# Performance work log

Hardware: AMD Instinct MI355X
Metric: run time of the kernel (lower is better)

Reference implementation:

```python
import jax, jax.numpy as jnp
import numpy as np

N_NODES = 50000
EPS = 1e-5


def sage_conv_max(x, src, dst, W_l, b_l, W_r):
    # PyG SAGEConv(aggr='max'): out = lin_l(max_j x_j) + lin_r(x_i)
    msg = x[src]                                   # [E, d] gather
    agg = jnp.full((x.shape[0], x.shape[1]), -jnp.inf, dtype=x.dtype)
    agg = agg.at[dst].max(msg)                     # scatter-max over edges
    agg = jnp.where(jnp.isneginf(agg), 0.0, agg)   # isolated nodes -> 0 (PyG convention)
    return agg @ W_l.T + b_l + x @ W_r.T


def batch_norm(x, gamma, beta):
    mean = jnp.mean(x, axis=0)
    var = jnp.var(x, axis=0)
    return (x - mean) * jax.lax.rsqrt(var + EPS) * gamma + beta


def setup_inputs() -> dict:
    key = jax.random.key(0)
    ks = jax.random.split(key, 10)
    d_in, d_h, d_out = 128, 128, 32
    s = lambda fan: 1.0 / np.sqrt(fan)
    return {
        "x": jax.random.normal(ks[0], (N_NODES, d_in), dtype=jnp.float32),
        "edge_index": jax.random.randint(ks[1], (2, 800000), 0, N_NODES, dtype=jnp.int32),
        "W_l1": jax.random.uniform(ks[2], (d_h, d_in), jnp.float32, -s(d_in), s(d_in)),
        "b_l1": jnp.zeros((d_h,), jnp.float32),
        "W_r1": jax.random.uniform(ks[3], (d_h, d_in), jnp.float32, -s(d_in), s(d_in)),
        "gamma1": jnp.ones((d_h,), jnp.float32),
        "beta1": jnp.zeros((d_h,), jnp.float32),
        "W_l2": jax.random.uniform(ks[4], (d_out, d_h), jnp.float32, -s(d_h), s(d_h)),
        "b_l2": jnp.zeros((d_out,), jnp.float32),
        "W_r2": jax.random.uniform(ks[5], (d_out, d_h), jnp.float32, -s(d_h), s(d_h)),
    }


def reference(x, edge_index, W_l1, b_l1, W_r1, gamma1, beta1, W_l2, b_l2, W_r2):
    src, dst = edge_index[0], edge_index[1]
    h = sage_conv_max(x, src, dst, W_l1, b_l1, W_r1)
    h = batch_norm(h, gamma1, beta1)
    h = jax.nn.relu(h)
    # dropout is identity at inference
    return sage_conv_max(h, src, dst, W_l2, b_l2, W_r2)
```

## Files before the change

kernel.cpp:

```cpp
#include <hip/hip_runtime.h>
#include <math.h>
#include <float.h>

#define N_NODES 50000
#define N_EDGES 800000
#define DH 128
#define NB 196
#define EB 4096
#define NBUCK 98
#define BSH 9
#define NTOT (NBUCK * NB)

typedef __attribute__((ext_vector_type(8))) short bf16x8;
typedef __attribute__((ext_vector_type(4))) float f32x4;

static __device__ __forceinline__ unsigned short f2bf(float f) {
  unsigned int u = __float_as_uint(f);
  u = (u + 0x7fff + ((u >> 16) & 1)) >> 16;
  return (unsigned short)u;
}

__global__ __launch_bounds__(256) void part_hist(const int* __restrict__ dst,
                                                 int* __restrict__ histT) {
  __shared__ int lh[NBUCK];
  const int tid = threadIdx.x, blk = blockIdx.x;
  if (tid < NBUCK) lh[tid] = 0;
  __syncthreads();
#pragma unroll
  for (int it = 0; it < EB / 256; ++it) {
    int e = blk * EB + it * 256 + tid;
    if (e < N_EDGES) atomicAdd(&lh[dst[e] >> BSH], 1);
  }
  __syncthreads();
  if (tid < NBUCK) histT[tid * NB + blk] = lh[tid];
}

__global__ __launch_bounds__(1024) void part_scan(int* __restrict__ histT) {
  const int PER = (NTOT + 1023) / 1024;
  int t = threadIdx.x;
  int v[(NTOT + 1023) / 1024];
  int base_i = t * PER;
  int mysum = 0;
#pragma unroll
  for (int i = 0; i < PER; ++i) {
    int idx = base_i + i;
    v[i] = (idx < NTOT) ? histT[idx] : 0;
    mysum += v[i];
  }
  __shared__ int s[1024];
  s[t] = mysum;
  __syncthreads();
  for (int off = 1; off < 1024; off <<= 1) {
    int x = (t >= off) ? s[t - off] : 0;
    __syncthreads();
    s[t] += x;
    __syncthreads();
  }
  int run = s[t] - mysum;
#pragma unroll
  for (int i = 0; i < PER; ++i) {
    int idx = base_i + i;
    if (idx < NTOT) histT[idx] = run;
    run += v[i];
  }
}

__global__ __launch_bounds__(256) void part_scatter(const int* __restrict__ src,
                                                    const int* __restrict__ dst,
                                                    const int* __restrict__ basesT,
                                                    unsigned int* __restrict__ pairs) {
  __shared__ int cur[NBUCK];
  const int tid = threadIdx.x, blk = blockIdx.x;
  if (tid < NBUCK) cur[tid] = basesT[tid * NB + blk];
  __syncthreads();
#pragma unroll
  for (int it = 0; it < EB / 256; ++it) {
    int e = blk * EB + it * 256 + tid;
    if (e < N_EDGES) {
      int d = dst[e];
      int p = atomicAdd(&cur[d >> BSH], 1);
      pairs[p] = (unsigned)src[e] | ((unsigned)(d & 511) << 16);
    }
  }
}

__global__ __launch_bounds__(1024) void bucket_sort(const unsigned int* __restrict__ pairs,
                                                    const int* __restrict__ basesT,
                                                    int* __restrict__ row_ptr,
                                                    int* __restrict__ elist) {
  __shared__ int hist[512], sc[512], cpos[512];
  const int b = blockIdx.x, tid = threadIdx.x;
  const int p0 = basesT[b * NB];
  const int p1 = (b < NBUCK - 1) ? basesT[(b + 1) * NB] : N_EDGES;
  if (tid < 512) hist[tid] = 0;
  __syncthreads();
  for (int p = p0 + tid; p < p1; p += 1024)
    atomicAdd(&hist[(pairs[p] >> 16) & 511], 1);
  __syncthreads();
  if (tid < 512) sc[tid] = hist[tid];
  __syncthreads();
  for (int off = 1; off < 512; off <<= 1) {
    int x = (tid < 512 && tid >= off) ? sc[tid - off] : 0;
    __syncthreads();
    if (tid < 512) sc[tid] += x;
    __syncthreads();
  }
  if (tid < 512) {
    int excl = sc[tid] - hist[tid];
    cpos[tid] = excl;
    int node = (b << BSH) + tid;
    if (node <= N_NODES) row_ptr[node] = p0 + excl;
  }
  __syncthreads();
  for (int p = p0 + tid; p < p1; p += 1024) {
    unsigned int pr = pairs[p];
    int loc = atomicAdd(&cpos[(pr >> 16) & 511], 1);
    elist[p0 + loc] = (int)(pr & 0xffffu);
  }
}

__global__ __launch_bounds__(256) void convert_all(
    const float* __restrict__ x, const float* __restrict__ Wl1,
    const float* __restrict__ Wr1, const float* __restrict__ Wl2,
    const float* __restrict__ Wr2, unsigned int* __restrict__ x_bf,
    unsigned short* __restrict__ Wcat1, unsigned short* __restrict__ Wcat2) {
  int b = blockIdx.x;
  if (b < 6250) {
    int i = b * 256 + threadIdx.x;
    float4 v = ((const float4*)x)[i];
    uint2 o;
    o.x = (unsigned int)f2bf(v.x) | ((unsigned int)f2bf(v.y) << 16);
    o.y = (unsigned int)f2bf(v.z) | ((unsigned int)f2bf(v.w) << 16);
    ((uint2*)x_bf)[i] = o;
  } else {
    int i = (b - 6250) * 256 + threadIdx.x;
    if (i < 32768) {
      int n = i >> 8, k = i & 255;
      float w = (k < 128) ? Wl1[n * 128 + k] : Wr1[n * 128 + (k - 128)];
      Wcat1[i] = f2bf(w);
    } else if (i < 40960) {
      int j = i - 32768;
      int n = j >> 8, k = j & 255;
      float w = (k < 128) ? Wl2[n * 128 + k] : Wr2[n * 128 + (k - 128)];
      Wcat2[j] = f2bf(w);
    }
  }
}

template <bool BN>
__global__ __launch_bounds__(256) void agg_max_bf16(const uint4* __restrict__ feat4,
                                                    const int* __restrict__ row_ptr,
                                                    const int* __restrict__ elist,
                                                    const float* __restrict__ gsums,
                                                    const float* __restrict__ gamma,
                                                    const float* __restrict__ beta,
                                                    uint4* __restrict__ out4) {
  __shared__ float s_scale[128], s_shift[128];
  if (BN) {
    int t = threadIdx.x;
    if (t < 128) {
      float sm = 0.f, sq = 0.f;
#pragma unroll
      for (int r = 0; r < 8; ++r) {
        sm += gsums[r * 256 + t];
        sq += gsums[r * 256 + 128 + t];
      }
      const float inv = 1.f / (float)N_NODES;
      float mean = sm * inv;
      float var = sq * inv - mean * mean;
      float sc = gamma[t] * rsqrtf(var + 1e-5f);
      s_scale[t] = sc;
      s_shift[t] = beta[t] - mean * sc;
    }
    __syncthreads();
  }

  int node = blockIdx.x * 4 + (threadIdx.x >> 6);
  int lane = threadIdx.x & 63;
  int eslot = lane >> 4;
  int fq = lane & 15;
  int e0 = row_ptr[node];
  int e1 = row_ptr[node + 1];
  float m[8];
#pragma unroll
  for (int j = 0; j < 8; ++j) m[j] = -FLT_MAX;

  if (e0 < e1) {
    const int last = e1 - 1;
    for (int base = e0; base < e1; base += 16) {
      int idx[4];
#pragma unroll
      for (int q = 0; q < 4; ++q) {
        int e = base + q * 4 + eslot;
        if (e > last) e = last;
        idx[q] = elist[e];
      }
      uint4 v[4];
#pragma unroll
      for (int q = 0; q < 4; ++q) v[q] = feat4[(size_t)idx[q] * 16 + fq];
#pragma unroll
      for (int q = 0; q < 4; ++q) {
        const unsigned int* pv = (const unsigned int*)&v[q];
#pragma unroll
        for (int c = 0; c < 4; ++c) {
          m[2 * c]     = fmaxf(m[2 * c],     __uint_as_float(pv[c] << 16));
          m[2 * c + 1] = fmaxf(m[2 * c + 1], __uint_as_float(pv[c] & 0xffff0000u));
        }
      }
    }
  }

#pragma unroll
  for (int j = 0; j < 8; ++j) {
    m[j] = fmaxf(m[j], __shfl_xor(m[j], 16, 64));
    m[j] = fmaxf(m[j], __shfl_xor(m[j], 32, 64));
  }
  if (eslot == 0) {
    if (e0 == e1) {
#pragma unroll
      for (int j = 0; j < 8; ++j) m[j] = 0.f;
    } else if (BN) {
#pragma unroll
      for (int j = 0; j < 8; ++j) {
        int col = fq * 8 + j;
        m[j] = fmaxf(m[j] * s_scale[col] + s_shift[col], 0.f);
      }
    }
    uint4 o;
    o.x = (__float_as_uint(m[0]) >> 16) | (__float_as_uint(m[1]) & 0xffff0000u);
    o.y = (__float_as_uint(m[2]) >> 16) | (__float_as_uint(m[3]) & 0xffff0000u);
    o.z = (__float_as_uint(m[4]) >> 16) | (__float_as_uint(m[5]) & 0xffff0000u);
    o.w = (__float_as_uint(m[6]) >> 16) | (__float_as_uint(m[7]) & 0xffff0000u);
    out4[(size_t)node * 16 + fq] = o;
  }
}

#define ASTR 264

template <int NT, bool BF16OUT, bool STATS, bool BNIN>
__global__ __launch_bounds__(256) void gemm_mfma(
    const unsigned short* __restrict__ Aa, const unsigned short* __restrict__ Ab,
    const unsigned short* __restrict__ Wcat, const float* __restrict__ bias,
    unsigned short* __restrict__ outb, float* __restrict__ outf,
    float* __restrict__ gsums, const float* __restrict__ gamma,
    const float* __restrict__ beta, int N) {
  __shared__ unsigned short Alds[128 * ASTR];
  __shared__ float s_sum[128], s_sq[128];
  __shared__ float s_scale[128], s_shift[128];
  const int tid = threadIdx.x;
  const int rowBase = blockIdx.x * 128;

  if (STATS && tid < 128) { s_sum[tid] = 0.f; s_sq[tid] = 0.f; }
  if (BNIN) {
    if (tid < 128) {
      float sm = 0.f, sq = 0.f;
#pragma unroll
      for (int r = 0; r < 8; ++r) {
        sm += gsums[r * 256 + tid];
        sq += gsums[r * 256 + 128 + tid];
      }
      const float inv = 1.f / (float)N_NODES;
      float mean = sm * inv;
      float var = sq * inv - mean * mean;
      float sc = gamma[tid] * rsqrtf(var + 1e-5f);
      s_scale[tid] = sc;
      s_shift[tid] = beta[tid] - mean * sc;
    }
    __syncthreads();
  }

#pragma unroll
  for (int it = 0; it < 16; ++it) {
    int f = tid + it * 256;
    int r = f >> 5;
    int seg = f & 31;
    int n = rowBase + r;
    if (n >= N) n = N - 1;
    const unsigned short* src = (seg < 16)
        ? (Aa + (size_t)n * 128 + seg * 8)
        : (Ab + (size_t)n * 128 + (seg - 16) * 8);
    int4 d = *(const int4*)src;
    if (BNIN && seg >= 16) {
      int kb = (seg - 16) * 8;
      unsigned int* dp = (unsigned int*)&d;
#pragma unroll
      for (int c = 0; c < 4; ++c) {
        int k0 = kb + 2 * c;
        float lo = __uint_as_float(dp[c] << 16);
        float hi = __uint_as_float(dp[c] & 0xffff0000u);
        lo = fmaxf(lo * s_scale[k0] + s_shift[k0], 0.f);
        hi = fmaxf(hi * s_scale[k0 + 1] + s_shift[k0 + 1], 0.f);
        dp[c] = (unsigned)f2bf(lo) | ((unsigned)f2bf(hi) << 16);
      }
    }
    *(int4*)(&Alds[r * ASTR + seg * 8]) = d;
  }
  __syncthreads();

  const int wv = tid >> 6;
  const int lane = tid & 63;
  const int ln15 = lane & 15;
  const int quad = lane >> 4;
  const int m0 = wv * 32;

  f32x4 acc[2][NT] = {};

#pragma unroll
  for (int ks = 0; ks < 8; ++ks) {
    const int k0 = ks * 32;
    bf16x8 a0 = *(const bf16x8*)(&Alds[(m0 + ln15) * ASTR + k0 + quad * 8]);
    bf16x8 a1 = *(const bf16x8*)(&Alds[(m0 + 16 + ln15) * ASTR + k0 + quad * 8]);
#pragma unroll
    for (int nt = 0; nt < NT; ++nt) {
      bf16x8 b = *(const bf16x8*)(Wcat + (size_t)(nt * 16 + ln15) * 256 + k0 + quad * 8);
      acc[0][nt] = __builtin_amdgcn_mfma_f32_16x16x32_bf16(a0, b, acc[0][nt], 0, 0, 0);
      acc[1][nt] = __builtin_amdgcn_mfma_f32_16x16x32_bf16(a1, b, acc[1][nt], 0, 0, 0);
    }
  }

  const int ldo = NT * 16;
#pragma unroll
  for (int nt = 0; nt < NT; ++nt) {
    int col = nt * 16 + ln15;
    float bv = bias[col];
    float psum = 0.f, psq = 0.f;
#pragma unroll
    for (int mt = 0; mt < 2; ++mt) {
#pragma unroll
      for (int i = 0; i < 4; ++i) {
        int r = rowBase + m0 + mt * 16 + quad * 4 + i;
        if (r < N) {
          float val = acc[mt][nt][i] + bv;
          if (STATS) { psum += val; psq += val * val; }
          if (BF16OUT)
            outb[(size_t)r * ldo + col] = f2bf(val);
          else
            outf[(size_t)r * ldo + col] = val;
        }
      }
    }
    if (STATS) {
      atomicAdd(&s_sum[col], psum);
      atomicAdd(&s_sq[col], psq);
    }
  }
  if (STATS) {
    __syncthreads();
    if (tid < 128) {
      int rep = blockIdx.x & 7;
      atomicAdd(&gsums[rep * 256 + tid], s_sum[tid]);
      atomicAdd(&gsums[rep * 256 + 128 + tid], s_sq[tid]);
    }
  }
}

extern "C" void kernel_launch(void* const* d_in, const int* in_sizes, int n_in,
                              void* d_out, int out_size, void* d_ws, size_t ws_size,
                              hipStream_t stream) {
  (void)in_sizes; (void)n_in; (void)out_size; (void)ws_size;
  const float* x     = (const float*)d_in[0];
  const int*   eidx  = (const int*)d_in[1];
  const float* W_l1  = (const float*)d_in[2];
  const float* b_l1  = (const float*)d_in[3];
  const float* W_r1  = (const float*)d_in[4];
  const float* gamma = (const float*)d_in[5];
  const float* beta  = (const float*)d_in[6];
  const float* W_l2  = (const float*)d_in[7];
  const float* b_l2  = (const float*)d_in[8];
  const float* W_r2  = (const float*)d_in[9];
  const int* srcp = eidx;
  const int* dstp = eidx + N_EDGES;
  float* out = (float*)d_out;

  int* wsi = (int*)d_ws;
  float* gsums   = (float*)wsi;
  int*   histT   = wsi + 2048;
  int*   row_ptr = wsi + 21264;
  int*   elist   = wsi + 71268;
  unsigned int* pairs = (unsigned int*)(wsi + 871268);
  unsigned int* x_bf   = (unsigned int*)(wsi + 1671268);
  unsigned int* agg_bf = (unsigned int*)(wsi + 4871268);
  unsigned int* h_bf   = (unsigned int*)(wsi + 8071268);
  unsigned short* Wcat1 = (unsigned short*)(wsi + 11271268);
  unsigned short* Wcat2 = (unsigned short*)(wsi + 11287652);

  hipMemsetAsync(gsums, 0, 2048 * 4, stream);

  part_hist<<<dim3(NB), 256, 0, stream>>>(dstp, histT);
  part_scan<<<dim3(1), 1024, 0, stream>>>(histT);
  part_scatter<<<dim3(NB), 256, 0, stream>>>(srcp, dstp, histT, pairs);
  bucket_sort<<<dim3(NBUCK), 1024, 0, stream>>>(pairs, histT, row_ptr, elist);

  convert_all<<<dim3(6410), 256, 0, stream>>>(x, W_l1, W_r1, W_l2, W_r2,
                                              x_bf, Wcat1, Wcat2);

  agg_max_bf16<false><<<dim3(N_NODES / 4), 256, 0, stream>>>(
      (const uint4*)x_bf, row_ptr, elist, nullptr, nullptr, nullptr, (uint4*)agg_bf);
  gemm_mfma<8, true, true, false><<<dim3(391), 256, 0, stream>>>(
      (const unsigned short*)agg_bf, (const unsigned short*)x_bf, Wcat1, b_l1,
      (unsigned short*)h_bf, nullptr, gsums, nullptr, nullptr, N_NODES);

  agg_max_bf16<true><<<dim3(N_NODES / 4), 256, 0, stream>>>(
      (const uint4*)h_bf, row_ptr, elist, gsums, gamma, beta, (uint4*)agg_bf);
  gemm_mfma<2, false, false, true><<<dim3(391), 256, 0, stream>>>(
      (const unsigned short*)agg_bf, (const unsigned short*)h_bf, Wcat2, b_l2,
      nullptr, out, gsums, gamma, beta, N_NODES);
}
```

Measured before the change: 250.3 us.

## Fuse max aggregation into MFMA GEMM and merge setup kernels

Each GEMM block now computes the neighbour max-aggregation for its 128 rows and writes the result directly into shared memory, so the intermediate aggregated buffer is no longer written and re-read. The histogram, bf16 conversion and gsums zeroing are combined into one setup kernel, which removes a memset and several launches. The trade-off is that the gather work now runs on only 391 blocks of 512 threads, each wave handling 16 nodes in sequence, which lowers parallelism and latency hiding for the irregular gather. The aggregated values are also now rounded to bf16 instead of truncated.

```diff
diff --git a/kernel.cpp b/kernel.cpp
--- a/kernel.cpp
+++ b/kernel.cpp
@@ -20,19 +20,48 @@
   return (unsigned short)u;
 }
 
-__global__ __launch_bounds__(256) void part_hist(const int* __restrict__ dst,
-                                                 int* __restrict__ histT) {
-  __shared__ int lh[NBUCK];
-  const int tid = threadIdx.x, blk = blockIdx.x;
-  if (tid < NBUCK) lh[tid] = 0;
-  __syncthreads();
-#pragma unroll
-  for (int it = 0; it < EB / 256; ++it) {
-    int e = blk * EB + it * 256 + tid;
-    if (e < N_EDGES) atomicAdd(&lh[dst[e] >> BSH], 1);
-  }
-  __syncthreads();
-  if (tid < NBUCK) histT[tid * NB + blk] = lh[tid];
+__global__ __launch_bounds__(256) void setup_kernel(
+    const int* __restrict__ dst, int* __restrict__ histT,
+    const float* __restrict__ x, const float* __restrict__ Wl1,
+    const float* __restrict__ Wr1, const float* __restrict__ Wl2,
+    const float* __restrict__ Wr2, unsigned int* __restrict__ x_bf,
+    unsigned short* __restrict__ Wcat1, unsigned short* __restrict__ Wcat2,
+    float* __restrict__ gsums) {
+  const int b = blockIdx.x, tid = threadIdx.x;
+  if (b < NB) {
+    __shared__ int lh[NBUCK];
+    if (tid < NBUCK) lh[tid] = 0;
+    __syncthreads();
+#pragma unroll
+    for (int it = 0; it < EB / 256; ++it) {
+      int e = b * EB + it * 256 + tid;
+      if (e < N_EDGES) atomicAdd(&lh[dst[e] >> BSH], 1);
+    }
+    __syncthreads();
+    if (tid < NBUCK) histT[tid * NB + b] = lh[tid];
+  } else if (b < NB + 6250) {
+    int i = (b - NB) * 256 + tid;
+    float4 v = ((const float4*)x)[i];
+    uint2 o;
+    o.x = (unsigned int)f2bf(v.x) | ((unsigned int)f2bf(v.y) << 16);
+    o.y = (unsigned int)f2bf(v.z) | ((unsigned int)f2bf(v.w) << 16);
+    ((uint2*)x_bf)[i] = o;
+  } else if (b < NB + 6410) {
+    int i = (b - NB - 6250) * 256 + tid;
+    if (i < 32768) {
+      int n = i >> 8, k = i & 255;
+      float w = (k < 128) ? Wl1[n * 128 + k] : Wr1[n * 128 + (k - 128)];
+      Wcat1[i] = f2bf(w);
+    } else if (i < 40960) {
+      int j = i - 32768;
+      int n = j >> 8, k = j & 255;
+      float w = (k < 128) ? Wl2[n * 128 + k] : Wr2[n * 128 + (k - 128)];
+      Wcat2[j] = f2bf(w);
+    }
+  } else {
+#pragma unroll
+    for (int i = 0; i < 8; ++i) gsums[i * 256 + tid] = 0.f;
+  }
 }
 
 __global__ __launch_bounds__(1024) void part_scan(int* __restrict__ histT) {
@@ -119,127 +148,13 @@
   }
 }
 
-__global__ __launch_bounds__(256) void convert_all(
-    const float* __restrict__ x, const float* __restrict__ Wl1,
-    const float* __restrict__ Wr1, const float* __restrict__ Wl2,
-    const float* __restrict__ Wr2, unsigned int* __restrict__ x_bf,
-    unsigned short* __restrict__ Wcat1, unsigned short* __restrict__ Wcat2) {
-  int b = blockIdx.x;
-  if (b < 6250) {
-    int i = b * 256 + threadIdx.x;
-    float4 v = ((const float4*)x)[i];
-    uint2 o;
-    o.x = (unsigned int)f2bf(v.x) | ((unsigned int)f2bf(v.y) << 16);
-    o.y = (unsigned int)f2bf(v.z) | ((unsigned int)f2bf(v.w) << 16);
-    ((uint2*)x_bf)[i] = o;
-  } else {
-    int i = (b - 6250) * 256 + threadIdx.x;
-    if (i < 32768) {
-      int n = i >> 8, k = i & 255;
-      float w = (k < 128) ? Wl1[n * 128 + k] : Wr1[n * 128 + (k - 128)];
-      Wcat1[i] = f2bf(w);
-    } else if (i < 40960) {
-      int j = i - 32768;
-      int n = j >> 8, k = j & 255;
-      float w = (k < 128) ? Wl2[n * 128 + k] : Wr2[n * 128 + (k - 128)];
-      Wcat2[j] = f2bf(w);
-    }
-  }
-}
-
-template <bool BN>
-__global__ __launch_bounds__(256) void agg_max_bf16(const uint4* __restrict__ feat4,
-                                                    const int* __restrict__ row_ptr,
-                                                    const int* __restrict__ elist,
-                                                    const float* __restrict__ gsums,
-                                                    const float* __restrict__ gamma,
-                                                    const float* __restrict__ beta,
-                                                    uint4* __restrict__ out4) {
-  __shared__ float s_scale[128], s_shift[128];
-  if (BN) {
-    int t = threadIdx.x;
-    if (t < 128) {
-      float sm = 0.f, sq = 0.f;
-#pragma unroll
-      for (int r = 0; r < 8; ++r) {
-        sm += gsums[r * 256 + t];
-        sq += gsums[r * 256 + 128 + t];
-      }
-      const float inv = 1.f / (float)N_NODES;
-      float mean = sm * inv;
-      float var = sq * inv - mean * mean;
-      float sc = gamma[t] * rsqrtf(var + 1e-5f);
-      s_scale[t] = sc;
-      s_shift[t] = beta[t] - mean * sc;
-    }
-    __syncthreads();
-  }
-
-  int node = blockIdx.x * 4 + (threadIdx.x >> 6);
-  int lane = threadIdx.x & 63;
-  int eslot = lane >> 4;
-  int fq = lane & 15;
-  int e0 = row_ptr[node];
-  int e1 = row_ptr[node + 1];
-  float m[8];
-#pragma unroll
-  for (int j = 0; j < 8; ++j) m[j] = -FLT_MAX;
-
-  if (e0 < e1) {
-    const int last = e1 - 1;
-    for (int base = e0; base < e1; base += 16) {
-      int idx[4];
-#pragma unroll
-      for (int q = 0; q < 4; ++q) {
-        int e = base + q * 4 + eslot;
-        if (e > last) e = last;
-        idx[q] = elist[e];
-      }
-      uint4 v[4];
-#pragma unroll
-      for (int q = 0; q < 4; ++q) v[q] = feat4[(size_t)idx[q] * 16 + fq];
-#pragma unroll
-      for (int q = 0; q < 4; ++q) {
-        const unsigned int* pv = (const unsigned int*)&v[q];
-#pragma unroll
-        for (int c = 0; c < 4; ++c) {
-          m[2 * c]     = fmaxf(m[2 * c],     __uint_as_float(pv[c] << 16));
-          m[2 * c + 1] = fmaxf(m[2 * c + 1], __uint_as_float(pv[c] & 0xffff0000u));
-        }
-      }
-    }
-  }
-
-#pragma unroll
-  for (int j = 0; j < 8; ++j) {
-    m[j] = fmaxf(m[j], __shfl_xor(m[j], 16, 64));
-    m[j] = fmaxf(m[j], __shfl_xor(m[j], 32, 64));
-  }
-  if (eslot == 0) {
-    if (e0 == e1) {
-#pragma unroll
-      for (int j = 0; j < 8; ++j) m[j] = 0.f;
-    } else if (BN) {
-#pragma unroll
-      for (int j = 0; j < 8; ++j) {
-        int col = fq * 8 + j;
-        m[j] = fmaxf(m[j] * s_scale[col] + s_shift[col], 0.f);
-      }
-    }
-    uint4 o;
-    o.x = (__float_as_uint(m[0]) >> 16) | (__float_as_uint(m[1]) & 0xffff0000u);
-    o.y = (__float_as_uint(m[2]) >> 16) | (__float_as_uint(m[3]) & 0xffff0000u);
-    o.z = (__float_as_uint(m[4]) >> 16) | (__float_as_uint(m[5]) & 0xffff0000u);
-    o.w = (__float_as_uint(m[6]) >> 16) | (__float_as_uint(m[7]) & 0xffff0000u);
-    out4[(size_t)node * 16 + fq] = o;
-  }
-}
-
 #define ASTR 264
 
 template <int NT, bool BF16OUT, bool STATS, bool BNIN>
-__global__ __launch_bounds__(256) void gemm_mfma(
-    const unsigned short* __restrict__ Aa, const unsigned short* __restrict__ Ab,
+__global__ __launch_bounds__(512) void fused_gemm(
+    const uint4* __restrict__ feat4,
+    const unsigned short* __restrict__ Abp,
+    const int* __restrict__ row_ptr, const int* __restrict__ elist,
     const unsigned short* __restrict__ Wcat, const float* __restrict__ bias,
     unsigned short* __restrict__ outb, float* __restrict__ outf,
     float* __restrict__ gsums, const float* __restrict__ gamma,
@@ -270,18 +185,14 @@
   }
 
 #pragma unroll
-  for (int it = 0; it < 16; ++it) {
-    int f = tid + it * 256;
-    int r = f >> 5;
-    int seg = f & 31;
+  for (int it = 0; it < 4; ++it) {
+    int f = tid + it * 512;
+    int r = f >> 4, seg = f & 15;
     int n = rowBase + r;
     if (n >= N) n = N - 1;
-    const unsigned short* src = (seg < 16)
-        ? (Aa + (size_t)n * 128 + seg * 8)
-        : (Ab + (size_t)n * 128 + (seg - 16) * 8);
-    int4 d = *(const int4*)src;
-    if (BNIN && seg >= 16) {
-      int kb = (seg - 16) * 8;
+    int4 d = *(const int4*)(Abp + (size_t)n * 128 + seg * 8);
+    if (BNIN) {
+      int kb = seg * 8;
       unsigned int* dp = (unsigned int*)&d;
 #pragma unroll
       for (int c = 0; c < 4; ++c) {
@@ -293,28 +204,83 @@
         dp[c] = (unsigned)f2bf(lo) | ((unsigned)f2bf(hi) << 16);
       }
     }
-    *(int4*)(&Alds[r * ASTR + seg * 8]) = d;
-  }
-  __syncthreads();
-
-  const int wv = tid >> 6;
-  const int lane = tid & 63;
+    *(int4*)(&Alds[r * ASTR + 128 + seg * 8]) = d;
+  }
+
+  const int wv = tid >> 6, lane = tid & 63;
+  const int eslot = lane >> 4, fq = lane & 15;
+  for (int i = 0; i < 16; ++i) {
+    int rloc = wv + 8 * i;
+    int node = rowBase + rloc;
+    if (node >= N) node = N - 1;
+    int e0 = row_ptr[node];
+    int e1 = row_ptr[node + 1];
+    float m[8];
+#pragma unroll
+    for (int j = 0; j < 8; ++j) m[j] = -FLT_MAX;
+    if (e0 < e1) {
+      const int last = e1 - 1;
+      for (int base = e0; base < e1; base += 16) {
+        int idx[4];
+#pragma unroll
+        for (int q = 0; q < 4; ++q) {
+          int e = base + q * 4 + eslot;
+          if (e > last) e = last;
+          idx[q] = elist[e];
+        }
+        uint4 v[4];
+#pragma unroll
+        for (int q = 0; q < 4; ++q) v[q] = feat4[(size_t)idx[q] * 16 + fq];
+#pragma unroll
+        for (int q = 0; q < 4; ++q) {
+          const unsigned int* pv = (const unsigned int*)&v[q];
+#pragma unroll
+          for (int c = 0; c < 4; ++c) {
+            m[2 * c]     = fmaxf(m[2 * c],     __uint_as_float(pv[c] << 16));
+            m[2 * c + 1] = fmaxf(m[2 * c + 1], __uint_as_float(pv[c] & 0xffff0000u));
+          }
+        }
+      }
+    }
+#pragma unroll
+    for (int j = 0; j < 8; ++j) {
+      m[j] = fmaxf(m[j], __shfl_xor(m[j], 16, 64));
+      m[j] = fmaxf(m[j], __shfl_xor(m[j], 32, 64));
+    }
+    if (eslot == 0) {
+      if (e0 == e1) {
+#pragma unroll
+        for (int j = 0; j < 8; ++j) m[j] = 0.f;
+      } else if (BNIN) {
+#pragma unroll
+        for (int j = 0; j < 8; ++j) {
+          int col = fq * 8 + j;
+          m[j] = fmaxf(m[j] * s_scale[col] + s_shift[col], 0.f);
+        }
+      }
+      uint4 o;
+      o.x = (unsigned)f2bf(m[0]) | ((unsigned)f2bf(m[1]) << 16);
+      o.y = (unsigned)f2bf(m[2]) | ((unsigned)f2bf(m[3]) << 16);
+      o.z = (unsigned)f2bf(m[4]) | ((unsigned)f2bf(m[5]) << 16);
+      o.w = (unsigned)f2bf(m[6]) | ((unsigned)f2bf(m[7]) << 16);
+      *(uint4*)(&Alds[rloc * ASTR + fq * 8]) = o;
+    }
+  }
+  __syncthreads();
+
   const int ln15 = lane & 15;
   const int quad = lane >> 4;
-  const int m0 = wv * 32;
-
-  f32x4 acc[2][NT] = {};
-
+  const int m0 = wv * 16;
+
+  f32x4 acc[NT] = {};
 #pragma unroll
   for (int ks = 0; ks < 8; ++ks) {
     const int k0 = ks * 32;
-    bf16x8 a0 = *(const bf16x8*)(&Alds[(m0 + ln15) * ASTR + k0 + quad * 8]);
-    bf16x8 a1 = *(const bf16x8*)(&Alds[(m0 + 16 + ln15) * ASTR + k0 + quad * 8]);
+    bf16x8 a = *(const bf16x8*)(&Alds[(m0 + ln15) * ASTR + k0 + quad * 8]);
 #pragma unroll
     for (int nt = 0; nt < NT; ++nt) {
       bf16x8 b = *(const bf16x8*)(Wcat + (size_t)(nt * 16 + ln15) * 256 + k0 + quad * 8);
-      acc[0][nt] = __builtin_amdgcn_mfma_f32_16x16x32_bf16(a0, b, acc[0][nt], 0, 0, 0);
-      acc[1][nt] = __builtin_amdgcn_mfma_f32_16x16x32_bf16(a1, b, acc[1][nt], 0, 0, 0);
+      acc[nt] = __builtin_amdgcn_mfma_f32_16x16x32_bf16(a, b, acc[nt], 0, 0, 0);
     }
   }
 
@@ -325,18 +291,15 @@
     float bv = bias[col];
     float psum = 0.f, psq = 0.f;
 #pragma unroll
-    for (int mt = 0; mt < 2; ++mt) {
-#pragma unroll
-      for (int i = 0; i < 4; ++i) {
-        int r = rowBase + m0 + mt * 16 + quad * 4 + i;
-        if (r < N) {
-          float val = acc[mt][nt][i] + bv;
-          if (STATS) { psum += val; psq += val * val; }
-          if (BF16OUT)
-            outb[(size_t)r * ldo + col] = f2bf(val);
-          else
-            outf[(size_t)r * ldo + col] = val;
-        }
+    for (int i = 0; i < 4; ++i) {
+      int r = rowBase + m0 + quad * 4 + i;
+      if (r < N) {
+        float val = acc[nt][i] + bv;
+        if (STATS) { psum += val; psq += val * val; }
+        if (BF16OUT)
+          outb[(size_t)r * ldo + col] = f2bf(val);
+        else
+          outf[(size_t)r * ldo + col] = val;
       }
     }
     if (STATS) {
@@ -379,30 +342,21 @@
   int*   elist   = wsi + 71268;
   unsigned int* pairs = (unsigned int*)(wsi + 871268);
   unsigned int* x_bf   = (unsigned int*)(wsi + 1671268);
-  unsigned int* agg_bf = (unsigned int*)(wsi + 4871268);
-  unsigned int* h_bf   = (unsigned int*)(wsi + 8071268);
-  unsigned short* Wcat1 = (unsigned short*)(wsi + 11271268);
-  unsigned short* Wcat2 = (unsigned short*)(wsi + 11287652);
-
-  hipMemsetAsync(gsums, 0, 2048 * 4, stream);
-
-  part_hist<<<dim3(NB), 256, 0, stream>>>(dstp, histT);
+  unsigned int* h_bf   = (unsigned int*)(wsi + 4871268);
+  unsigned short* Wcat1 = (unsigned short*)(wsi + 8071268);
+  unsigned short* Wcat2 = (unsigned short*)(wsi + 8087652);
+
+  setup_kernel<<<dim3(NB + 6410 + 1), 256, 0, stream>>>(
+      dstp, histT, x, W_l1, W_r1, W_l2, W_r2, x_bf, Wcat1, Wcat2, gsums);
   part_scan<<<dim3(1), 1024, 0, stream>>>(histT);
   part_scatter<<<dim3(NB), 256, 0, stream>>>(srcp, dstp, histT, pairs);
   bucket_sort<<<dim3(NBUCK), 1024, 0, stream>>>(pairs, histT, row_ptr, elist);
 
-  convert_all<<<dim3(6410), 256, 0, stream>>>(x, W_l1, W_r1, W_l2, W_r2,
-                                              x_bf, Wcat1, Wcat2);
-
-  agg_max_bf16<false><<<dim3(N_NODES / 4), 256, 0, stream>>>(
-      (const uint4*)x_bf, row_ptr, elist, nullptr, nullptr, nullptr, (uint4*)agg_bf);
-  gemm_mfma<8, true, true, false><<<dim3(391), 256, 0, stream>>>(
-      (const unsigned short*)agg_bf, (const unsigned short*)x_bf, Wcat1, b_l1,
-      (unsigned short*)h_bf, nullptr, gsums, nullptr, nullptr, N_NODES);
-
-  agg_max_bf16<true><<<dim3(N_NODES / 4), 256, 0, stream>>>(
-      (const uint4*)h_bf, row_ptr, elist, gsums, gamma, beta, (uint4*)agg_bf);
-  gemm_mfma<2, false, false, true><<<dim3(391), 256, 0, stream>>>(
-      (const unsigned short*)agg_bf, (const unsigned short*)h_bf, Wcat2, b_l2,
-      nullptr, out, gsums, gamma, beta, N_NODES);
-}
+  fused_gemm<8, true, true, false><<<dim3(391), 512, 0, stream>>>(
+      (const uint4*)x_bf, (const unsigned short*)x_bf, row_ptr, elist,
+      Wcat1, b_l1, (unsigned short*)h_bf, nullptr, gsums, nullptr, nullptr, N_NODES);
+
+  fused_gemm<2, false, false, true><<<dim3(391), 512, 0, stream>>>(
+      (const uint4*)h_bf, (const unsigned short*)h_bf, row_ptr, elist,
+      Wcat2, b_l2, nullptr, out, gsums, gamma, beta, N_NODES);
+}
```

Measured after the change: 269.1 us. 7.5% more time.
